# Performance work log

Hardware: AMD Instinct MI355X
Metric: run time of the kernel (lower is better)

Reference implementation:

```python
import jax, jax.numpy as jnp
import numpy as np

HIDDEN = 2048
N_HEADS = 16
HEAD_DIM = HIDDEN // N_HEADS  # 128
ROTARY_DIM = 32
ROPE_BASE = 10000.0
NEG_INF = -10000.0  # matches torch code's additive mask constant


def setup_inputs() -> dict:
    key = jax.random.key(0)
    k1, k2, k3 = jax.random.split(key, 3)
    x = jax.random.normal(k1, (2, 2048, HIDDEN), dtype=jnp.float32)
    # scale weights like nn.Linear default init (uniform ~ 1/sqrt(fan_in))
    Wqkv_w = jax.random.normal(k2, (3 * HIDDEN, HIDDEN), dtype=jnp.float32) * (1.0 / np.sqrt(HIDDEN))
    Wqkv_b = jax.random.normal(k3, (3 * HIDDEN,), dtype=jnp.float32) * 0.01
    return {"x": x, "Wqkv_w": Wqkv_w, "Wqkv_b": Wqkv_b}


def _rope_cos_sin(seqlen, dtype):
    inv_freq = 1.0 / (ROPE_BASE ** (jnp.arange(0, ROTARY_DIM, 2, dtype=jnp.float32) / ROTARY_DIM))
    t = jnp.arange(seqlen, dtype=jnp.float32)
    freqs = jnp.outer(t, inv_freq)  # (S, ROTARY_DIM//2)
    return jnp.cos(freqs).astype(dtype), jnp.sin(freqs).astype(dtype)


def _apply_rotary(u, cos, sin):
    # u: (B, S, H, D); rotate first ROTARY_DIM dims, GPT-NeoX half-split style
    u_rot, u_pass = u[..., :ROTARY_DIM], u[..., ROTARY_DIM:]
    u1, u2 = u_rot[..., : ROTARY_DIM // 2], u_rot[..., ROTARY_DIM // 2 :]
    c = cos[None, :, None, :]  # (1, S, 1, ROTARY_DIM//2)
    s = sin[None, :, None, :]
    rot = jnp.concatenate([u1 * c - u2 * s, u1 * s + u2 * c], axis=-1)
    return jnp.concatenate([rot, u_pass], axis=-1)


def reference(x, Wqkv_w, Wqkv_b):
    B, S, _ = x.shape
    qkv = jnp.einsum("bse,oe->bso", x, Wqkv_w) + Wqkv_b  # (B, S, 3*H*D)
    qkv = qkv.reshape(B, S, 3, N_HEADS, HEAD_DIM)
    cos, sin = _rope_cos_sin(S, x.dtype)
    q = _apply_rotary(qkv[:, :, 0], cos, sin)
    k = _apply_rotary(qkv[:, :, 1], cos, sin)
    v = qkv[:, :, 2]
    scale = 1.0 / np.sqrt(HEAD_DIM)
    scores = jnp.einsum("bthd,bshd->bhts", q, k * scale)  # (B, H, T, S)
    causal_mask = jnp.triu(jnp.full((S, S), NEG_INF, dtype=scores.dtype), 1)
    scores = scores + causal_mask
    attn = jax.nn.softmax(scores, axis=-1)
    out = jnp.einsum("bhts,bshd->bthd", attn, v)  # (B, S, H, D)
    return out.reshape(B, S, N_HEADS * HEAD_DIM)
```

## Files before the change

kernel.cpp:

```cpp
#include <hip/hip_runtime.h>

#define B_    2
#define S_    2048
#define E_    2048
#define NH_   16
#define HD_   128
#define NQKV_ 6144
#define M_    4096
#define XN_   (M_ * E_)
#define NPAN  (E_ / 32)

typedef short bf16x8 __attribute__((ext_vector_type(8)));
typedef float f32x4  __attribute__((ext_vector_type(4)));

typedef const __attribute__((address_space(1))) void* gas_t;
typedef __attribute__((address_space(3))) void*       las_t;

__device__ inline float b2f(unsigned short u) {
    return __uint_as_float(((unsigned int)u) << 16);
}
__device__ inline unsigned short f2b(float f) {
    unsigned int x = __float_as_uint(f);
    x = x + 0x7fffu + ((x >> 16) & 1u);
    return (unsigned short)(x >> 16);
}
__device__ inline unsigned int pk2(float lo, float hi) {
    return (unsigned int)f2b(lo) | ((unsigned int)f2b(hi) << 16);
}

__global__ __launch_bounds__(256) void cvt_bf16(
    const float* __restrict__ X,
    const float* __restrict__ W,
    unsigned short* __restrict__ O)
{
    const long i = (long)(blockIdx.x * 256 + threadIdx.x) * 8;
    const float* src = (i < XN_) ? (X + i) : (W + (i - XN_));
    const float4 a = *(const float4*)(src);
    const float4 b = *(const float4*)(src + 4);
    uint4 o = { pk2(a.x, a.y), pk2(a.z, a.w), pk2(b.x, b.y), pk2(b.z, b.w) };
    *(uint4*)(O + i) = o;
}

__global__ __launch_bounds__(512, 4) void qkv_gemm(
    const unsigned short* __restrict__ Xb,
    const unsigned short* __restrict__ Wb,
    const float* __restrict__ bias,
    unsigned short* __restrict__ qb,
    unsigned short* __restrict__ kb,
    unsigned short* __restrict__ vt)
{
    union GS {
        struct {
            unsigned short As[3][128 * 32];
            unsigned short Bs[3][256 * 32];
        } s;
        unsigned short Eqk[128 * 264];
        unsigned short Ev [256 * 136];
    };
    __shared__ __align__(16) GS gs;

    const int t    = threadIdx.x;
    const int lane = t & 63;
    const int w    = t >> 6;
    const int wr   = w >> 2;
    const int wc   = w & 3;
    const int quad = (lane >> 4) & 3;
    const int l16  = lane & 15;

    const int xcd = (int)blockIdx.x & 7;
    const int j   = (int)blockIdx.x >> 3;
    const int m0  = (j / 3) * 128;
    const int n0  = (xcd * 3 + (j % 3)) * 256;

    auto stageA = [&](int p) {
        const int sl = p % 3;
        const int k0 = p * 32;
        const int ub  = w * 64;
        const int u   = ub + lane;
        const int row = u >> 2;
        const int ko  = (u & 3) ^ ((row >> 1) & 3);
        __builtin_amdgcn_global_load_lds(
            (gas_t)(Xb + (size_t)(m0 + row) * E_ + k0 + ko * 8),
            (las_t)&gs.s.As[sl][ub * 8], 16, 0, 0);
    };
    auto stageB = [&](int p) {
        const int sl = p % 3;
        const int k0 = p * 32;
        #pragma unroll
        for (int c = 0; c < 2; c++) {
            const int ub  = c * 512 + w * 64;
            const int u   = ub + lane;
            const int row = u >> 2;
            const int ko  = (u & 3) ^ ((row >> 1) & 3);
            __builtin_amdgcn_global_load_lds(
                (gas_t)(Wb + (size_t)(n0 + row) * E_ + k0 + ko * 8),
                (las_t)&gs.s.Bs[sl][ub * 8], 16, 0, 0);
        }
    };

    f32x4 acc[4][4];
    #pragma unroll
    for (int i = 0; i < 4; i++)
        #pragma unroll
        for (int j2 = 0; j2 < 4; j2++)
            #pragma unroll
            for (int r = 0; r < 4; r++) acc[i][j2][r] = 0.0f;

    stageA(0); stageB(0);
    stageA(1); stageB(1);
    asm volatile("s_waitcnt vmcnt(0)" ::: "memory");
    __builtin_amdgcn_s_barrier();

    for (int p = 0; p < NPAN; p++) {
        const int sl = p % 3;
        bf16x8 af[4], bfv[4];

        #pragma unroll
        for (int mf = 0; mf < 4; mf++) {
            const int row = wr * 64 + mf * 16 + l16;
            af[mf] = *(const bf16x8*)&gs.s.As[sl][row * 32 + (quad ^ ((row >> 1) & 3)) * 8];
        }
        #pragma unroll
        for (int nf = 0; nf < 4; nf++) {
            const int rb = wc * 64 + nf * 16 + l16;
            bfv[nf] = *(const bf16x8*)&gs.s.Bs[sl][rb * 32 + (quad ^ ((rb >> 1) & 3)) * 8];
        }

        if (p + 2 < NPAN) {
            stageA(p + 2); stageB(p + 2);
            asm volatile("s_waitcnt vmcnt(3)" ::: "memory");
        } else {
            asm volatile("s_waitcnt vmcnt(0)" ::: "memory");
        }
        __builtin_amdgcn_s_barrier();
        __builtin_amdgcn_s_setprio(1);
        #pragma unroll
        for (int mf = 0; mf < 4; mf++)
            #pragma unroll
            for (int nf = 0; nf < 4; nf++)
                acc[mf][nf] = __builtin_amdgcn_mfma_f32_16x16x32_bf16(
                    af[mf], bfv[nf], acc[mf][nf], 0, 0, 0);
        __builtin_amdgcn_s_setprio(0);
        __builtin_amdgcn_s_barrier();
    }

    const int which = n0 >> 11;

    float bv[4];
    #pragma unroll
    for (int nf = 0; nf < 4; nf++) bv[nf] = bias[n0 + wc * 64 + nf * 16 + l16];
    #pragma unroll
    for (int mi = 0; mi < 4; mi++)
        #pragma unroll
        for (int nf = 0; nf < 4; nf++)
            #pragma unroll
            for (int r = 0; r < 4; r++) acc[mi][nf][r] += bv[nf];

    if ((wc & 1) == 0 && which < 2) {
        const float inv = exp2f(-0.83048202372184059f * (float)l16);
        #pragma unroll
        for (int mi = 0; mi < 4; mi++) {
            #pragma unroll
            for (int r = 0; r < 4; r++) {
                const int m = m0 + wr * 64 + mi * 16 + quad * 4 + r;
                const int sdx = m & (S_ - 1);
                float c, sn;
                __sincosf((float)sdx * inv, &sn, &c);
                const float u1 = acc[mi][0][r], u2 = acc[mi][1][r];
                acc[mi][0][r] = u1 * c - u2 * sn;
                acc[mi][1][r] = u1 * sn + u2 * c;
            }
        }
    }

    const int hb = (n0 >> 7) & 15;
    const int bb = m0 >> 11;
    const int sb = m0 & (S_ - 1);
    if (which < 2) {
        unsigned short* dst = (which == 0) ? qb : kb;
        unsigned short* E = gs.Eqk;
        #pragma unroll
        for (int mi = 0; mi < 4; mi++) {
            const int m = wr * 64 + mi * 16 + quad * 4;
            #pragma unroll
            for (int nf = 0; nf < 4; nf++) {
                const int col = wc * 64 + nf * 16 + l16;
                #pragma unroll
                for (int r = 0; r < 4; r++)
                    E[(m + r) * 264 + col] = f2b(acc[mi][nf][r]);
            }
        }
        __syncthreads();
        const int em  = t >> 2;
        const int ecg = (t & 3) * 8;
        unsigned short* orow =
            dst + ((size_t)(bb * NH_ + hb) * S_ + sb + em) * HD_;
        #pragma unroll
        for (int i = 0; i < 8; i++) {
            const int chunk = ecg + i;
            const int hh = chunk >> 4;
            const int d  = (chunk & 15) * 8;
            uint4 vv = *(const uint4*)&E[em * 264 + chunk * 8];
            *(uint4*)&orow[(size_t)hh * (HD_ * S_) + d] = vv;
        }
    } else {
        unsigned short* E = gs.Ev;
        #pragma unroll
        for (int mi = 0; mi < 4; mi++) {
            const int m = wr * 64 + mi * 16 + quad * 4;
            #pragma unroll
            for (int nf = 0; nf < 4; nf++) {
                const int col = wc * 64 + nf * 16 + l16;
                #pragma unroll
                for (int r = 0; r < 4; r++)
                    E[col * 136 + m + r] = f2b(acc[mi][nf][r]);
            }
        }
        __syncthreads();
        const int col = t >> 1;
        const int cb  = (t & 1) * 8;
        const int hh  = hb + (col >> 7);
        const int d   = col & 127;
        unsigned short* vrow =
            vt + ((size_t)(bb * NH_ + hh) * HD_ + d) * S_ + sb;
        #pragma unroll
        for (int i = 0; i < 8; i++) {
            const int chunk = cb + i;
            uint4 vv = *(const uint4*)&E[col * 136 + chunk * 8];
            *(uint4*)&vrow[chunk * 8] = vv;
        }
    }
}

#define PSTR 72
#define OSTR 132

__global__ __launch_bounds__(256, 2) void attn_mfma(
    const unsigned short* __restrict__ qb,
    const unsigned short* __restrict__ kb,
    const unsigned short* __restrict__ vt,
    float* __restrict__ out)
{
    union SM {
        struct {
            unsigned short Ks[2][64 * 128];
            unsigned short Vs[2][128 * 64];
            unsigned short Ps[4 * 16 * PSTR];
        } a;
        float Ow[4 * 16 * OSTR];
    };
    __shared__ __align__(16) SM sm;

    const int bid  = blockIdx.x;
    const int qt   = 31 - (bid >> 5);
    const int bh   = bid & 31;
    const int b    = bh >> 4;
    const int h    = bh & 15;
    const int t    = threadIdx.x;
    const int lane = t & 63;
    const int w    = t >> 6;
    const int quad = lane >> 4;
    const int l16  = lane & 15;

    const int wrow0  = qt * 64 + w * 16;
    const int ntiles = qt + 1;

    unsigned short* Pw = sm.a.Ps + w * 16 * PSTR;

    const int ksrow = w * 4 + (lane >> 4);
    const int ksu   = lane & 15;
    const int vdrow = w * 8 + (lane >> 3);
    const int vsu   = lane & 7;

    auto stage = [&](int kt2, int bsel) {
        const int s2 = kt2 * 64;
        #pragma unroll
        for (int c = 0; c < 4; c++) {
            const int srow = c * 16 + ksrow;
            __builtin_amdgcn_global_load_lds(
                (gas_t)(kb + ((size_t)(bh * S_ + s2 + srow)) * HD_
                        + (ksu ^ (srow & 7)) * 8),
                (las_t)&sm.a.Ks[bsel][(c * 16 + w * 4) * 128], 16, 0, 0);
        }
        #pragma unroll
        for (int c = 0; c < 4; c++) {
            const int drow = c * 32 + vdrow;
            __builtin_amdgcn_global_load_lds(
                (gas_t)(vt + ((size_t)(bh * HD_ + drow)) * S_ + s2
                        + (vsu ^ (drow & 7)) * 8),
                (las_t)&sm.a.Vs[bsel][(c * 32 + w * 8) * 64], 16, 0, 0);
        }
    };

    bf16x8 qf[4];
    {
        const unsigned short* qp =
            qb + ((size_t)(bh * S_ + wrow0 + l16)) * HD_ + quad * 8;
        #pragma unroll
        for (int c = 0; c < 4; c++)
            qf[c] = *(const bf16x8*)(qp + c * 32);
    }

    f32x4 of[8];
    #pragma unroll
    for (int db = 0; db < 8; db++)
        #pragma unroll
        for (int r = 0; r < 4; r++) of[db][r] = 0.0f;
    float mr[4], lr[4];
    #pragma unroll
    for (int r = 0; r < 4; r++) { mr[r] = -1e30f; lr[r] = 0.0f; }

    const float scale2 = 0.12751744459892879f;
    const float mneg2  = -14426.950408889634f;

    stage(0, 0);
    __syncthreads();
    int cur = 0;

    for (int kt = 0; kt < ntiles; kt++) {
        const int s0 = kt * 64;
        if (kt + 1 < ntiles) stage(kt + 1, cur ^ 1);

        f32x4 sf[4];
        #pragma unroll
        for (int nb = 0; nb < 4; nb++)
            #pragma unroll
            for (int r = 0; r < 4; r++) sf[nb][r] = 0.0f;
        #pragma unroll
        for (int c = 0; c < 4; c++) {
            #pragma unroll
            for (int nb = 0; nb < 4; nb++) {
                const int u = (c * 4 + quad) ^ (l16 & 7);
                bf16x8 kf = *(const bf16x8*)
                    &sm.a.Ks[cur][(nb * 16 + l16) * 128 + u * 8];
                sf[nb] = __builtin_amdgcn_mfma_f32_16x16x32_bf16(
                    qf[c], kf, sf[nb], 0, 0, 0);
            }
        }

        const bool need_mask = (s0 + 63 > wrow0);
        {
            const int qr0 = wrow0 + quad * 4;
            #pragma unroll
            for (int nb = 0; nb < 4; nb++) {
                const int kcol = s0 + nb * 16 + l16;
                #pragma unroll
                for (int r = 0; r < 4; r++) {
                    float s = sf[nb][r] * scale2;
                    if (need_mask && kcol > qr0 + r) s += mneg2;
                    sf[nb][r] = s;
                }
            }
        }

        {
            float mt4[4];
            #pragma unroll
            for (int r = 0; r < 4; r++) {
                float mt = fmaxf(fmaxf(sf[0][r], sf[1][r]),
                                 fmaxf(sf[2][r], sf[3][r]));
                mt = fmaxf(mt, __shfl_xor(mt, 1));
                mt = fmaxf(mt, __shfl_xor(mt, 2));
                mt = fmaxf(mt, __shfl_xor(mt, 4));
                mt = fmaxf(mt, __shfl_xor(mt, 8));
                mt4[r] = mt;
            }
            const bool grew = (mt4[0] > mr[0]) || (mt4[1] > mr[1]) ||
                              (mt4[2] > mr[2]) || (mt4[3] > mr[3]);
            if (__any(grew)) {
                float alpha[4];
                #pragma unroll
                for (int r = 0; r < 4; r++) {
                    const float mnew = fmaxf(mr[r], mt4[r]);
                    alpha[r] = __builtin_amdgcn_exp2f(mr[r] - mnew);
                    mr[r] = mnew;
                    lr[r] *= alpha[r];
                }
                #pragma unroll
                for (int db = 0; db < 8; db++)
                    #pragma unroll
                    for (int r = 0; r < 4; r++) of[db][r] *= alpha[r];
            }
            #pragma unroll
            for (int r = 0; r < 4; r++) {
                float rs = 0.0f;
                #pragma unroll
                for (int nb = 0; nb < 4; nb++) {
                    float p = __builtin_amdgcn_exp2f(sf[nb][r] - mr[r]);
                    sf[nb][r] = p;
                    rs += p;
                }
                lr[r] += rs;
            }

            #pragma unroll
            for (int nb = 0; nb < 4; nb++)
                #pragma unroll
                for (int r = 0; r < 4; r++)
                    Pw[(quad * 4 + r) * PSTR + nb * 16 + l16] = f2b(sf[nb][r]);
        }

        #pragma unroll
        for (int kc = 0; kc < 2; kc++) {
            bf16x8 pf = *(const bf16x8*)&Pw[l16 * PSTR + kc * 32 + quad * 8];
            #pragma unroll
            for (int db = 0; db < 8; db++) {
                const int u = (kc * 4 + quad) ^ (l16 & 7);
                bf16x8 vf = *(const bf16x8*)
                    &sm.a.Vs[cur][(db * 16 + l16) * 64 + u * 8];
                of[db] = __builtin_amdgcn_mfma_f32_16x16x32_bf16(
                    pf, vf, of[db], 0, 0, 0);
            }
        }

        __syncthreads();
        cur ^= 1;
    }

    float* Ow = sm.Ow + w * 16 * OSTR;
    float inv[4];
    #pragma unroll
    for (int r = 0; r < 4; r++) {
        float ls = lr[r];
        ls += __shfl_xor(ls, 1);
        ls += __shfl_xor(ls, 2);
        ls += __shfl_xor(ls, 4);
        ls += __shfl_xor(ls, 8);
        inv[r] = 1.0f / ls;
    }
    #pragma unroll
    for (int db = 0; db < 8; db++)
        #pragma unroll
        for (int r = 0; r < 4; r++)
            Ow[(quad * 4 + r) * OSTR + db * 16 + l16] = of[db][r] * inv[r];
    #pragma unroll
    for (int rg = 0; rg < 4; rg++) {
        const int rowl = rg * 4 + quad;
        float* op = out + ((size_t)(b * S_ + wrow0 + rowl)) * E_ + h * HD_;
        #pragma unroll
        for (int u = 0; u < 2; u++) {
            float4 v4 = *(const float4*)&Ow[rowl * OSTR + u * 64 + l16 * 4];
            *(float4*)(op + u * 64 + l16 * 4) = v4;
        }
    }
}

extern "C" void kernel_launch(void* const* d_in, const int* in_sizes, int n_in,
                              void* d_out, int out_size, void* d_ws, size_t ws_size,
                              hipStream_t stream)
{
    const float* x    = (const float*)d_in[0];
    const float* W    = (const float*)d_in[1];
    const float* bias = (const float*)d_in[2];
    float* out = (float*)d_out;

    const size_t per = (size_t)B_ * NH_ * S_ * HD_;
    unsigned short* qb = (unsigned short*)d_ws;
    unsigned short* kb = qb + per;
    unsigned short* vt = kb + per;
    unsigned short* Xb = vt + per;
    unsigned short* Wb = Xb + (size_t)XN_;

    const int cvt_elems = XN_ + NQKV_ * E_;
    cvt_bf16<<<cvt_elems / (256 * 8), 256, 0, stream>>>(x, W, Xb);

    dim3 gemm_grid((M_ / 128) * (NQKV_ / 256));
    qkv_gemm<<<gemm_grid, 512, 0, stream>>>(Xb, Wb, bias, qb, kb, vt);

    attn_mfma<<<dim3(32 * 32), 256, 0, stream>>>(qb, kb, vt, out);
}
```

Measured before the change: 318.0 us.

## Replace LDS double buffer with register prefetch to raise attention occupancy

Attention K/V tiles are no longer double-buffered in LDS through direct global-to-LDS loads. The next tile is now prefetched into registers during compute and written to a single LDS buffer after a barrier. Halving the LDS footprint and raising launch bounds to three blocks per CU is meant to improve occupancy and latency hiding. In exchange it adds a second barrier per iteration, uses more VGPRs for the staging registers under a tighter register cap, and may spill.

```diff
diff --git a/kernel.cpp b/kernel.cpp
--- a/kernel.cpp
+++ b/kernel.cpp
@@ -235,7 +235,7 @@
 #define PSTR 72
 #define OSTR 132
 
-__global__ __launch_bounds__(256, 2) void attn_mfma(
+__global__ __launch_bounds__(256, 3) void attn_mfma(
     const unsigned short* __restrict__ qb,
     const unsigned short* __restrict__ kb,
     const unsigned short* __restrict__ vt,
@@ -243,8 +243,8 @@
 {
     union SM {
         struct {
-            unsigned short Ks[2][64 * 128];
-            unsigned short Vs[2][128 * 64];
+            unsigned short Ks[64 * 128];
+            unsigned short Vs[128 * 64];
             unsigned short Ps[4 * 16 * PSTR];
         } a;
         float Ow[4 * 16 * OSTR];
@@ -267,29 +267,28 @@
 
     unsigned short* Pw = sm.a.Ps + w * 16 * PSTR;
 
-    const int ksrow = w * 4 + (lane >> 4);
-    const int ksu   = lane & 15;
-    const int vdrow = w * 8 + (lane >> 3);
-    const int vsu   = lane & 7;
-
-    auto stage = [&](int kt2, int bsel) {
+    const int krow = t >> 2, kub = (t & 3) * 4;
+    const int vdrow = t >> 1, vub = (t & 1) * 4;
+
+    uint4 kr[4], vr[4];
+    auto load_tile = [&](int kt2) {
         const int s2 = kt2 * 64;
-        #pragma unroll
-        for (int c = 0; c < 4; c++) {
-            const int srow = c * 16 + ksrow;
-            __builtin_amdgcn_global_load_lds(
-                (gas_t)(kb + ((size_t)(bh * S_ + s2 + srow)) * HD_
-                        + (ksu ^ (srow & 7)) * 8),
-                (las_t)&sm.a.Ks[bsel][(c * 16 + w * 4) * 128], 16, 0, 0);
-        }
-        #pragma unroll
-        for (int c = 0; c < 4; c++) {
-            const int drow = c * 32 + vdrow;
-            __builtin_amdgcn_global_load_lds(
-                (gas_t)(vt + ((size_t)(bh * HD_ + drow)) * S_ + s2
-                        + (vsu ^ (drow & 7)) * 8),
-                (las_t)&sm.a.Vs[bsel][(c * 32 + w * 8) * 64], 16, 0, 0);
-        }
+        const unsigned short* kg =
+            kb + ((size_t)(bh * S_ + s2 + krow)) * HD_ + kub * 8;
+        #pragma unroll
+        for (int u = 0; u < 4; u++) kr[u] = *(const uint4*)(kg + u * 8);
+        const unsigned short* vg =
+            vt + ((size_t)(bh * HD_ + vdrow)) * S_ + s2 + vub * 8;
+        #pragma unroll
+        for (int u = 0; u < 4; u++) vr[u] = *(const uint4*)(vg + u * 8);
+    };
+    auto write_tile = [&]() {
+        #pragma unroll
+        for (int u = 0; u < 4; u++)
+            *(uint4*)&sm.a.Ks[krow * 128 + ((kub + u) ^ (krow & 7)) * 8] = kr[u];
+        #pragma unroll
+        for (int u = 0; u < 4; u++)
+            *(uint4*)&sm.a.Vs[vdrow * 64 + ((vub + u) ^ (vdrow & 7)) * 8] = vr[u];
     };
 
     bf16x8 qf[4];
@@ -313,13 +312,13 @@
     const float scale2 = 0.12751744459892879f;
     const float mneg2  = -14426.950408889634f;
 
-    stage(0, 0);
+    load_tile(0);
+    write_tile();
     __syncthreads();
-    int cur = 0;
 
     for (int kt = 0; kt < ntiles; kt++) {
         const int s0 = kt * 64;
-        if (kt + 1 < ntiles) stage(kt + 1, cur ^ 1);
+        if (kt + 1 < ntiles) load_tile(kt + 1);
 
         f32x4 sf[4];
         #pragma unroll
@@ -332,7 +331,7 @@
             for (int nb = 0; nb < 4; nb++) {
                 const int u = (c * 4 + quad) ^ (l16 & 7);
                 bf16x8 kf = *(const bf16x8*)
-                    &sm.a.Ks[cur][(nb * 16 + l16) * 128 + u * 8];
+                    &sm.a.Ks[(nb * 16 + l16) * 128 + u * 8];
                 sf[nb] = __builtin_amdgcn_mfma_f32_16x16x32_bf16(
                     qf[c], kf, sf[nb], 0, 0, 0);
             }
@@ -407,14 +406,17 @@
             for (int db = 0; db < 8; db++) {
                 const int u = (kc * 4 + quad) ^ (l16 & 7);
                 bf16x8 vf = *(const bf16x8*)
-                    &sm.a.Vs[cur][(db * 16 + l16) * 64 + u * 8];
+                    &sm.a.Vs[(db * 16 + l16) * 64 + u * 8];
                 of[db] = __builtin_amdgcn_mfma_f32_16x16x32_bf16(
                     pf, vf, of[db], 0, 0, 0);
             }
         }
 
         __syncthreads();
-        cur ^= 1;
+        if (kt + 1 < ntiles) {
+            write_tile();
+            __syncthreads();
+        }
     }
 
     float* Ow = sm.Ow + w * 16 * OSTR;
```

After: 416.0 us. 1.31x slower.
